# Kernel optimization log

Measured on AMD Instinct MI355X. Metric: run time of the kernel, lower is better.

Reference implementation:

```python
import jax, jax.numpy as jnp
import numpy as np


def setup_inputs() -> dict:
    key = jax.random.key(0)
    k1, k2, k3, k4 = jax.random.split(key, 4)
    B, CIN, H, W = 4, 64, 512, 512
    COUT, K, WDIM = 64, 3, 512
    x = jax.random.normal(k1, (B, CIN, H, W), jnp.float32)
    w = jax.random.normal(k2, (B, WDIM), jnp.float32)
    # init_std = 1/lrmul = 1.0 for both weights (lrmul=1)
    conv_w = jax.random.normal(k3, (K, K, CIN, COUT), jnp.float32)
    mod_w = jax.random.normal(k4, (WDIM, CIN), jnp.float32)
    mod_b = jnp.zeros((CIN,), jnp.float32)
    return {"x": x, "w": w, "conv_w": conv_w, "mod_w": mod_w, "mod_b": mod_b}


def reference(x, w, conv_w, mod_w, mod_b):
    B, Cin, H, W_ = x.shape
    K, _, _, Cout = conv_w.shape
    wdim = mod_w.shape[0]
    # Dense (gain=1, lrmul=1): runtime_coef = 1/sqrt(fan_in)
    rc_dense = np.float32(1.0 / np.sqrt(wdim))
    # BiasAct linear (lrmul=1, gain=1): just add bias; then +1.0
    style = w @ (rc_dense * mod_w) + mod_b + 1.0  # [B, Cin]
    # conv weight runtime coef (gain=1, lrmul=1)
    rc_conv = np.float32(1.0 / np.sqrt(K * K * Cin))
    # per-sample modulated weight [B, K, K, Cin, Cout]
    wt = (rc_conv * conv_w)[None] * style[:, None, None, :, None]
    # demodulate over (kh, kw, Cin)
    d = jax.lax.rsqrt(jnp.sum(wt * wt, axis=(1, 2, 3)) + 1e-8)  # [B, Cout]
    wt = wt * d[:, None, None, None, :]
    # transpose to [K, K, Cin, B, Cout] and fold batch into output channels
    wt = jnp.transpose(wt, (1, 2, 3, 0, 4)).reshape(K, K, Cin, B * Cout)
    # grouped conv: groups = B
    xg = x.reshape(1, B * Cin, H, W_)
    out = jax.lax.conv_general_dilated(
        xg, wt,
        window_strides=(1, 1),
        padding="SAME",
        dimension_numbers=("NCHW", "HWIO", "NCHW"),
        feature_group_count=B,
    )
    return out.reshape(B, Cout, H, W_)
```

## Files before the change

kernel.cpp:

```cpp
#include <hip/hip_runtime.h>


typedef __bf16 bf16x8 __attribute__((ext_vector_type(8)));
typedef float f32x4 __attribute__((ext_vector_type(4)));
typedef unsigned short ushortx8 __attribute__((ext_vector_type(8)));

#define CIN   64
#define COUT  64
#define HH    512
#define WW    512
#define WDIM  512

#define TILE_H 8
#define TILE_W 32
#define XR     10
#define XC     34
#define CPAD   72

__device__ __forceinline__ unsigned short f2bf(float f) {
    unsigned int u = __float_as_uint(f);
    unsigned int r = (u + 0x7FFFu + ((u >> 16) & 1u)) >> 16;
    return (unsigned short)r;
}

__global__ void prep_kernel(const float* __restrict__ wv,
                            const float* __restrict__ conv_w,
                            const float* __restrict__ mod_w,
                            const float* __restrict__ mod_b,
                            unsigned short* __restrict__ Wswz) {
    const int b    = blockIdx.x;
    const int tid  = threadIdx.x;
    const int lane6 = tid & 63;
    const int part  = tid >> 6;
    __shared__ float red[256];
    __shared__ float style[64];
    __shared__ float dsc[64];
    const float rc_dense = 0.04419417382415922f;
    const float rc_conv  = 0.041666666666666664f;

    float s = 0.f;
    const float* wb = wv + b * WDIM;
    for (int k = part * 128; k < part * 128 + 128; ++k)
        s += wb[k] * mod_w[k * 64 + lane6];
    red[tid] = s;
    __syncthreads();
    if (part == 0) {
        float tot = red[lane6] + red[64 + lane6] + red[128 + lane6] + red[192 + lane6];
        style[lane6] = tot * rc_dense + mod_b[lane6] + 1.0f;
    }
    __syncthreads();

    float qq = 0.f;
    for (int idx = part * 144; idx < part * 144 + 144; ++idx) {
        float v = conv_w[idx * 64 + lane6] * style[idx & 63];
        qq += v * v;
    }
    red[tid] = qq;
    __syncthreads();
    if (part == 0) {
        float tot = red[lane6] + red[64 + lane6] + red[128 + lane6] + red[192 + lane6];
        dsc[lane6] = rsqrtf(rc_conv * rc_conv * tot + 1e-8f);
    }
    __syncthreads();

    for (int it = 0; it < 18; ++it) {
        int id  = it * 256 + tid;
        int l   = id & 63;
        int mf  = (id >> 6) & 3;
        int ks  = (id >> 8) & 1;
        int t   = id >> 9;
        int co  = mf * 16 + (l & 15);
        int ci0 = ks * 32 + (l >> 4) * 8;
        float fco = rc_conv * dsc[co];
        ushortx8 ov;
#pragma unroll
        for (int j = 0; j < 8; ++j) {
            int ci = ci0 + j;
            float v = conv_w[(t * 64 + ci) * 64 + co] * style[ci] * fco;
            ov[j] = f2bf(v);
        }
        *reinterpret_cast<ushortx8*>(Wswz + (size_t)b * 36864 + id * 8) = ov;
    }
}

__global__ __launch_bounds__(256, 3) void conv_kernel(
        const float* __restrict__ x,
        const unsigned short* __restrict__ Wswz,
        float* __restrict__ out) {
    __shared__ unsigned short xs[XR * XC * CPAD];

    const int tid  = threadIdx.x;
    const int blk  = blockIdx.x;
    const int b    = blk >> 10;
    const int tile = blk & 1023;
    const int tr   = tile >> 4;
    const int tc   = tile & 15;
    const int h0   = tr * TILE_H;
    const int w0   = tc * TILE_W;
    const float* xb = x + (size_t)b * CIN * HH * WW;

    for (int it = 0; it < 11; ++it) {
        int id = it * 256 + tid;
        if (id < 2720) {
            int c   = id % 34;
            int rem = id / 34;
            int r   = rem % 10;
            int o8  = rem / 10;
            int rg  = h0 + r - 1;
            int cg  = w0 + c - 1;
            ushortx8 v;
            if (((unsigned)rg < (unsigned)HH) && ((unsigned)cg < (unsigned)WW)) {
                const float* p = xb + ((size_t)(o8 * 8) * HH + rg) * WW + cg;
#pragma unroll
                for (int j = 0; j < 8; ++j)
                    v[j] = f2bf(p[(size_t)j * HH * WW]);
            } else {
#pragma unroll
                for (int j = 0; j < 8; ++j) v[j] = 0;
            }
            *reinterpret_cast<ushortx8*>(&xs[(r * XC + c) * CPAD + o8 * 8]) = v;
        }
    }
    __syncthreads();

    const int l   = tid & 63;
    const int wv  = tid >> 6;
    const int m16 = l & 15;
    const int q   = l >> 4;

    f32x4 acc[4][4];
#pragma unroll
    for (int mf = 0; mf < 4; ++mf)
#pragma unroll
        for (int nf = 0; nf < 4; ++nf)
            acc[mf][nf] = (f32x4){0.f, 0.f, 0.f, 0.f};

    int Xbase[4];
#pragma unroll
    for (int nf = 0; nf < 4; ++nf) {
        int np = (wv * 4 + nf) * 16 + m16;
        int pr = np >> 5, pc = np & 31;
        Xbase[nf] = (pr * XC + pc) * CPAD + q * 8;
    }
    const unsigned short* Wb = Wswz + (size_t)b * 36864 + l * 8;

    for (int kh = 0; kh < 3; ++kh) {
        for (int kw = 0; kw < 3; ++kw) {
            int t = kh * 3 + kw;
#pragma unroll
            for (int s = 0; s < 2; ++s) {
                const unsigned short* Wt = Wb + (t * 2 + s) * 2048;
                bf16x8 a[4], bb[4];
#pragma unroll
                for (int mf = 0; mf < 4; ++mf)
                    a[mf] = *reinterpret_cast<const bf16x8*>(Wt + mf * 512);
                int so = (kh * XC + kw) * CPAD + s * 32;
#pragma unroll
                for (int nf = 0; nf < 4; ++nf)
                    bb[nf] = *reinterpret_cast<const bf16x8*>(&xs[Xbase[nf] + so]);
#pragma unroll
                for (int mf = 0; mf < 4; ++mf)
#pragma unroll
                    for (int nf = 0; nf < 4; ++nf)
                        acc[mf][nf] = __builtin_amdgcn_mfma_f32_16x16x32_bf16(
                            a[mf], bb[nf], acc[mf][nf], 0, 0, 0);
            }
        }
    }

    float* ob = out + (size_t)b * COUT * HH * WW;
#pragma unroll
    for (int nf = 0; nf < 4; ++nf) {
        int np = (wv * 4 + nf) * 16 + m16;
        int pr = np >> 5, pc = np & 31;
        int h = h0 + pr, wc = w0 + pc;
#pragma unroll
        for (int mf = 0; mf < 4; ++mf) {
            int co = mf * 16 + q * 4;
            float* po = ob + ((size_t)co * HH + h) * WW + wc;
#pragma unroll
            for (int reg = 0; reg < 4; ++reg)
                po[(size_t)reg * HH * WW] = acc[mf][nf][reg];
        }
    }
}

extern "C" void kernel_launch(void* const* d_in, const int* in_sizes, int n_in,
                              void* d_out, int out_size, void* d_ws, size_t ws_size,
                              hipStream_t stream) {
    const float* x      = (const float*)d_in[0];
    const float* w      = (const float*)d_in[1];
    const float* conv_w = (const float*)d_in[2];
    const float* mod_w  = (const float*)d_in[3];
    const float* mod_b  = (const float*)d_in[4];
    float* out = (float*)d_out;
    unsigned short* Wswz = (unsigned short*)d_ws;

    prep_kernel<<<4, 256, 0, stream>>>(w, conv_w, mod_w, mod_b, Wswz);
    conv_kernel<<<4096, 256, 0, stream>>>(x, Wswz, out);
}
```

Before: 545.2 us.

## Vectorize input tile loads with float4 and split weight prep across more blocks

The input halo load now has each thread read four consecutive columns for four channels with 128-bit float4 loads, instead of scalar strided loads of eight channels per pixel. Each transposed column is packed into a 4-channel bf16 store to LDS, and the starting column is rotated by thread id to spread bank conflicts; the LDS row pitch grows from 34 to 36 columns to match the 4-aligned load. The prep kernel is split across 36 blocks (batch x tap) so the weight swizzle runs in parallel, though each block recomputes style and demodulation. The change costs more LDS per block and extra redundant prep arithmetic.

```diff
diff --git a/kernel.cpp b/kernel.cpp
--- a/kernel.cpp
+++ b/kernel.cpp
@@ -4,6 +4,7 @@
 typedef __bf16 bf16x8 __attribute__((ext_vector_type(8)));
 typedef float f32x4 __attribute__((ext_vector_type(4)));
 typedef unsigned short ushortx8 __attribute__((ext_vector_type(8)));
+typedef unsigned short ushortx4 __attribute__((ext_vector_type(4)));
 
 #define CIN   64
 #define COUT  64
@@ -14,7 +15,7 @@
 #define TILE_H 8
 #define TILE_W 32
 #define XR     10
-#define XC     34
+#define XC     36
 #define CPAD   72
 
 __device__ __forceinline__ unsigned short f2bf(float f) {
@@ -28,7 +29,8 @@
                             const float* __restrict__ mod_w,
                             const float* __restrict__ mod_b,
                             unsigned short* __restrict__ Wswz) {
-    const int b    = blockIdx.x;
+    const int b    = blockIdx.x / 9;
+    const int t    = blockIdx.x % 9;
     const int tid  = threadIdx.x;
     const int lane6 = tid & 63;
     const int part  = tid >> 6;
@@ -63,12 +65,11 @@
     }
     __syncthreads();
 
-    for (int it = 0; it < 18; ++it) {
-        int id  = it * 256 + tid;
-        int l   = id & 63;
-        int mf  = (id >> 6) & 3;
-        int ks  = (id >> 8) & 1;
-        int t   = id >> 9;
+    for (int it = 0; it < 2; ++it) {
+        int id2 = it * 256 + tid;
+        int l   = id2 & 63;
+        int mf  = (id2 >> 6) & 3;
+        int ks  = id2 >> 8;
         int co  = mf * 16 + (l & 15);
         int ci0 = ks * 32 + (l >> 4) * 8;
         float fco = rc_conv * dsc[co];
@@ -76,10 +77,9 @@
 #pragma unroll
         for (int j = 0; j < 8; ++j) {
             int ci = ci0 + j;
-            float v = conv_w[(t * 64 + ci) * 64 + co] * style[ci] * fco;
-            ov[j] = f2bf(v);
-        }
-        *reinterpret_cast<ushortx8*>(Wswz + (size_t)b * 36864 + id * 8) = ov;
+            ov[j] = f2bf(conv_w[(t * 64 + ci) * 64 + co] * style[ci] * fco);
+        }
+        *reinterpret_cast<ushortx8*>(Wswz + (size_t)b * 36864 + ((size_t)t * 512 + id2) * 8) = ov;
     }
 }
 
@@ -99,26 +99,48 @@
     const int w0   = tc * TILE_W;
     const float* xb = x + (size_t)b * CIN * HH * WW;
 
-    for (int it = 0; it < 11; ++it) {
+    for (int it = 0; it < 7; ++it) {
         int id = it * 256 + tid;
-        if (id < 2720) {
-            int c   = id % 34;
-            int rem = id / 34;
-            int r   = rem % 10;
-            int o8  = rem / 10;
-            int rg  = h0 + r - 1;
-            int cg  = w0 + c - 1;
-            ushortx8 v;
-            if (((unsigned)rg < (unsigned)HH) && ((unsigned)cg < (unsigned)WW)) {
-                const float* p = xb + ((size_t)(o8 * 8) * HH + rg) * WW + cg;
-#pragma unroll
-                for (int j = 0; j < 8; ++j)
-                    v[j] = f2bf(p[(size_t)j * HH * WW]);
-            } else {
-#pragma unroll
-                for (int j = 0; j < 8; ++j) v[j] = 0;
+        if (id >= 1600) break;
+        int cq  = id % 10;
+        int rem = id / 10;
+        int r   = rem % 10;
+        int ciq = rem / 10;
+        int rg  = h0 + r - 1;
+        int cg0 = w0 + cq * 4 - 4;
+        float va[4][4];
+        if ((unsigned)rg < (unsigned)HH) {
+#pragma unroll
+            for (int k = 0; k < 4; ++k) {
+                const float* p = xb + ((size_t)(ciq * 4 + k) * HH + rg) * WW;
+                if (cg0 >= 0 && cg0 + 3 < WW) {
+                    f32x4 v4 = *reinterpret_cast<const f32x4*>(p + cg0);
+#pragma unroll
+                    for (int j = 0; j < 4; ++j) va[k][j] = v4[j];
+                } else {
+#pragma unroll
+                    for (int j = 0; j < 4; ++j) {
+                        int cg = cg0 + j;
+                        va[k][j] = ((unsigned)cg < (unsigned)WW) ? p[cg] : 0.f;
+                    }
+                }
             }
-            *reinterpret_cast<ushortx8*>(&xs[(r * XC + c) * CPAD + o8 * 8]) = v;
+        } else {
+#pragma unroll
+            for (int k = 0; k < 4; ++k)
+#pragma unroll
+                for (int j = 0; j < 4; ++j) va[k][j] = 0.f;
+        }
+#pragma unroll
+        for (int jj = 0; jj < 4; ++jj) {
+            int j = (jj + tid) & 3;
+            int c = cq * 4 + j - 3;
+            if ((unsigned)c < (unsigned)XC) {
+                ushortx4 pk;
+#pragma unroll
+                for (int k = 0; k < 4; ++k) pk[k] = f2bf(va[k][j]);
+                *reinterpret_cast<ushortx4*>(&xs[(r * XC + c) * CPAD + ciq * 4]) = pk;
+            }
         }
     }
     __syncthreads();
@@ -196,6 +218,6 @@
     float* out = (float*)d_out;
     unsigned short* Wswz = (unsigned short*)d_ws;
 
-    prep_kernel<<<4, 256, 0, stream>>>(w, conv_w, mod_w, mod_b, Wswz);
+    prep_kernel<<<36, 256, 0, stream>>>(w, conv_w, mod_w, mod_b, Wswz);
     conv_kernel<<<4096, 256, 0, stream>>>(x, Wswz, out);
 }
```

Measured after the change: 608.6 us. 11.6% more time.
